# Performance work log

Hardware: AMD Instinct MI355X
Metric: run time of the kernel (lower is better)

Reference implementation:

```python
import jax, jax.numpy as jnp
import numpy as np

B, N, D = 2, 2048, 768
H = 12
DH = D // H
SCALE = DH ** -0.5


def setup_inputs() -> dict:
    key = jax.random.key(0)
    k1, k2, k3 = jax.random.split(key, 3)
    x = jax.random.normal(k1, (B, N, D), dtype=jnp.float32)
    w_qkv = jax.random.normal(k2, (D, 3 * D), dtype=jnp.float32) * (D ** -0.5)
    b_qkv = jnp.zeros((3 * D,), dtype=jnp.float32)
    w_proj = jax.random.normal(k3, (D, D), dtype=jnp.float32) * (D ** -0.5)
    b_proj = jnp.zeros((D,), dtype=jnp.float32)
    return {"x": x, "w_qkv": w_qkv, "b_qkv": b_qkv, "w_proj": w_proj, "b_proj": b_proj}


def reference(x, w_qkv, b_qkv, w_proj, b_proj):
    b, n, d = x.shape
    # qkv: (B, n, 3, H, DH) -> (3, B, H, n, DH)
    qkv = (x @ w_qkv + b_qkv).reshape(b, n, 3, H, DH).transpose(2, 0, 3, 1, 4)
    q, k, v = qkv[0], qkv[1], qkv[2]
    # naive full attention matrix (B, H, n, n)
    attn = jnp.einsum('bhqd,bhkd->bhqk', q, k) * SCALE
    attn = jax.nn.softmax(attn, axis=-1)
    out = jnp.einsum('bhqk,bhkd->bhqd', attn, v)  # (B, H, n, DH)
    out = out.transpose(0, 2, 1, 3).reshape(b, n, d)
    return out @ w_proj + b_proj
```

## Files before the change

### kernel.cpp

```cpp
#include <hip/hip_runtime.h>


#define CB 2
#define CN 2048
#define CD 768
#define CH 12
#define CDH 64
#define CEXPSCALE 0.18033688f

typedef __bf16 bf16x8 __attribute__((ext_vector_type(8)));
typedef float f32x4 __attribute__((ext_vector_type(4)));
typedef unsigned short u16x8 __attribute__((ext_vector_type(8)));

static __device__ __forceinline__ unsigned short f2bf(float f) {
  union { float f; unsigned u; } v; v.f = f;
  unsigned r = v.u + 0x7fffu + ((v.u >> 16) & 1u);
  return (unsigned short)(r >> 16);
}

static __device__ __forceinline__ void gld_lds16(const unsigned short* g, unsigned short* lds_base) {
  __builtin_amdgcn_global_load_lds(
      (const __attribute__((address_space(1))) unsigned int*)g,
      (__attribute__((address_space(3))) unsigned int*)(unsigned int)(unsigned long long)lds_base,
      16, 0, 0);
}

__global__ __launch_bounds__(256) void prep(const float* __restrict__ x,
                                            unsigned short* __restrict__ xb,
                                            const float* __restrict__ w_qkv,
                                            unsigned short* __restrict__ wqkv_t,
                                            const float* __restrict__ w_proj,
                                            unsigned short* __restrict__ wproj_t) {
  __shared__ __align__(16) unsigned short t[64][72];
  const int bid = blockIdx.x, tid = threadIdx.x;
#pragma unroll
  for (int it = 0; it < 2; ++it) {
    size_t i = ((size_t)(bid * 2 + it) * 256 + tid) * 8;
    f32x4 a = *(const f32x4*)&x[i];
    f32x4 b = *(const f32x4*)&x[i + 4];
    u16x8 o;
#pragma unroll
    for (int j = 0; j < 4; ++j) { o[j] = f2bf(a[j]); o[4 + j] = f2bf(b[j]); }
    *(u16x8*)&xb[i] = o;
  }
  if (bid >= 576) return;
  const float* src; unsigned short* dst; int R, C, c0, r0;
  if (bid < 432) { src = w_qkv; dst = wqkv_t; R = 768; C = 2304; c0 = (bid % 36) * 64; r0 = (bid / 36) * 64; }
  else { int u = bid - 432; src = w_proj; dst = wproj_t; R = 768; C = 768; c0 = (u % 12) * 64; r0 = (u / 12) * 64; }
#pragma unroll
  for (int i = 0; i < 4; ++i) {
    int c = tid + i * 256;
    int row = c >> 4, cc = (c & 15) * 4;
    f32x4 v = *(const f32x4*)&src[(size_t)(r0 + row) * C + c0 + cc];
#pragma unroll
    for (int j = 0; j < 4; ++j) t[row][cc + j] = f2bf(v[j]);
  }
  __syncthreads();
#pragma unroll
  for (int i = 0; i < 2; ++i) {
    int c = tid + i * 256;
    int drow = c >> 3, rc = (c & 7) * 8;
    u16x8 v;
#pragma unroll
    for (int j = 0; j < 8; ++j) v[j] = t[rc + j][drow];
    *(u16x8*)&dst[(size_t)(c0 + drow) * R + r0 + rc] = v;
  }
}

extern __shared__ __align__(16) unsigned short smem[];

template <int TM, int TN>
__global__ __launch_bounds__(256, 4) void gemm_db(const unsigned short* __restrict__ A,
                                                  const unsigned short* __restrict__ Bt,
                                                  const float* __restrict__ bias,
                                                  int M, int N, int K, int mode,
                                                  unsigned short* __restrict__ o0,
                                                  unsigned short* __restrict__ o1,
                                                  unsigned short* __restrict__ o2,
                                                  float* __restrict__ outF) {
  constexpr int NT = TN / 32;
  unsigned short* As = smem;
  unsigned short* Bs = smem + 2 * TM * 32;
  unsigned short* Ct = smem;
  const int tid = threadIdx.x;
  const int w = tid >> 6, lane = tid & 63, quad = lane >> 4, lc = lane & 15;
  const int wm = (w >> 1) * 32, wn = (w & 1) * (TN / 2);
  const int row0 = blockIdx.y * TM, col0 = blockIdx.x * TN;
  f32x4 acc[2][NT] = {};

  const int rl = lane >> 2, cl = lane & 3;
  const int gc = cl ^ ((rl >> 1) & 3);
  const int rsw = (lc >> 1) & 3;
  const int nk = K / 32;

  auto stage = [&](int kt, int buf) {
    const int k0 = kt * 32;
    gld_lds16(&A[(size_t)(row0 + w * 16 + rl) * K + k0 + gc * 8],
              &As[buf * (TM * 32) + (w * 16) * 32]);
#pragma unroll
    for (int jb = 0; jb < TN / 64; ++jb)
      gld_lds16(&Bt[(size_t)(col0 + w * (TN / 4) + jb * 16 + rl) * K + k0 + gc * 8],
                &Bs[buf * (TN * 32) + (w * (TN / 4) + jb * 16) * 32]);
  };

  stage(0, 0);
  for (int kt = 0; kt < nk; ++kt) {
    const int bb = kt & 1;
    __syncthreads();
    if (kt + 1 < nk) stage(kt + 1, bb ^ 1);
    bf16x8 af[2], bfv[NT];
#pragma unroll
    for (int mt = 0; mt < 2; ++mt)
      af[mt] = *(const bf16x8*)&As[bb * (TM * 32) + (wm + mt * 16 + lc) * 32 + (quad ^ rsw) * 8];
#pragma unroll
    for (int nt = 0; nt < NT; ++nt)
      bfv[nt] = *(const bf16x8*)&Bs[bb * (TN * 32) + (wn + nt * 16 + lc) * 32 + (quad ^ rsw) * 8];
#pragma unroll
    for (int mt = 0; mt < 2; ++mt)
#pragma unroll
      for (int nt = 0; nt < NT; ++nt)
        acc[mt][nt] = __builtin_amdgcn_mfma_f32_16x16x32_bf16(af[mt], bfv[nt], acc[mt][nt], 0, 0, 0);
  }

  if (mode == 0 && col0 >= 1536) {
    __syncthreads();
#pragma unroll
    for (int mt = 0; mt < 2; ++mt) {
#pragma unroll
      for (int nt = 0; nt < NT; ++nt) {
        int jl = wn + nt * 16 + lc;
        int il0 = wm + mt * 16 + quad * 4;
        float bj = bias[col0 + jl];
        unsigned short a0 = f2bf(acc[mt][nt][0] + bj);
        unsigned short a1 = f2bf(acc[mt][nt][1] + bj);
        unsigned short a2 = f2bf(acc[mt][nt][2] + bj);
        unsigned short a3 = f2bf(acc[mt][nt][3] + bj);
        uint2 dd;
        dd.x = (unsigned)a0 | ((unsigned)a1 << 16);
        dd.y = (unsigned)a2 | ((unsigned)a3 << 16);
        *(uint2*)&Ct[jl * (TM + 8) + il0] = dd;
      }
    }
    __syncthreads();
    const int b = row0 >> 11, n0 = row0 & 2047;
    constexpr int CPR = TM / 8;
#pragma unroll
    for (int i = 0; i < (TN * CPR) / 256; ++i) {
      int c = tid + i * 256;
      int jl = c / CPR, cc = (c % CPR) * 8;
      u16x8 v = *(const u16x8*)&Ct[jl * (TM + 8) + cc];
      int jcol = col0 - 1536 + jl;
      int h = jcol >> 6, d = jcol & 63;
      size_t gr = ((size_t)(b * CH + h) * CDH + d);
      *(u16x8*)&o2[gr * CN + n0 + cc] = v;
    }
  } else {
#pragma unroll
    for (int mt = 0; mt < 2; ++mt) {
#pragma unroll
      for (int nt = 0; nt < NT; ++nt) {
#pragma unroll
        for (int r = 0; r < 4; ++r) {
          int i = row0 + wm + mt * 16 + quad * 4 + r;
          int j = col0 + wn + nt * 16 + lc;
          float v = acc[mt][nt][r] + bias[j];
          if (mode == 0) {
            int b = i >> 11, n = i & 2047;
            int sec = (j >= 768) ? 1 : 0;
            int within = j - sec * 768;
            int h = within >> 6, d = within & 63;
            int bh = b * CH + h;
            if (sec == 0) o0[((size_t)bh * CN + n) * CDH + d] = f2bf(v * CEXPSCALE);
            else          o1[((size_t)bh * CN + n) * CDH + d] = f2bf(v);
          } else {
            outF[(size_t)i * N + j] = v;
          }
        }
      }
    }
  }
}

__global__ __launch_bounds__(256, 3) void attn64(const unsigned short* __restrict__ Q,
                                                 const unsigned short* __restrict__ K,
                                                 const unsigned short* __restrict__ Vt,
                                                 unsigned short* __restrict__ O) {
  __shared__ __align__(16) unsigned short Kls[2][64 * 64];
  __shared__ __align__(16) unsigned short Vls[2][64 * 64];
  __shared__ __align__(16) unsigned short P[4][16][88];
  const int bh = blockIdx.x, qt = blockIdx.y;
  const int tid = threadIdx.x;
  const int w = tid >> 6, lane = tid & 63, quad = lane >> 4, lc = lane & 15;
  const unsigned short* Qb = Q + (size_t)bh * CN * CDH;
  const unsigned short* Kb = K + (size_t)bh * CN * CDH;
  const unsigned short* Vb = Vt + (size_t)bh * CDH * CN;
  const int q0 = qt * 64 + w * 16;

  const int sr = lane >> 3, sc = lane & 7;
  const int sg = sc ^ sr;
  const int ksw = lc & 7;
  const int c0r = quad ^ ksw;
  const int c1r = c0r ^ 4;

  bf16x8 qf0 = *(const bf16x8*)&Qb[(size_t)(q0 + lc) * CDH + quad * 8];
  bf16x8 qf1 = *(const bf16x8*)&Qb[(size_t)(q0 + lc) * CDH + 32 + quad * 8];

  f32x4 o[4] = {};
  float rs = 0.f;

#pragma unroll
  for (int j2 = 0; j2 < 2; ++j2) {
    int j = w * 2 + j2;
    int r = j * 8 + sr;
    gld_lds16(&Kb[(size_t)r * CDH + sg * 8], &Kls[0][j * 8 * 64]);
    gld_lds16(&Vb[(size_t)r * CN + 0 + sg * 8], &Vls[0][j * 8 * 64]);
  }

  for (int kt = 0; kt < CN / 64; ++kt) {
    const int bb = kt & 1;
    __syncthreads();
    if (kt + 1 < CN / 64) {
      const int kn = (kt + 1) * 64;
#pragma unroll
      for (int j2 = 0; j2 < 2; ++j2) {
        int j = w * 2 + j2;
        int r = j * 8 + sr;
        gld_lds16(&Kb[(size_t)(kn + r) * CDH + sg * 8], &Kls[bb ^ 1][j * 8 * 64]);
        gld_lds16(&Vb[(size_t)r * CN + kn + sg * 8], &Vls[bb ^ 1][j * 8 * 64]);
      }
    }
#pragma unroll
    for (int t = 0; t < 4; ++t) {
      bf16x8 kf0 = *(const bf16x8*)&Kls[bb][(t * 16 + lc) * 64 + c0r * 8];
      bf16x8 kf1 = *(const bf16x8*)&Kls[bb][(t * 16 + lc) * 64 + c1r * 8];
      f32x4 z = {0.f, 0.f, 0.f, 0.f};
      z = __builtin_amdgcn_mfma_f32_16x16x32_bf16(kf0, qf0, z, 0, 0, 0);
      z = __builtin_amdgcn_mfma_f32_16x16x32_bf16(kf1, qf1, z, 0, 0, 0);
      float p0 = exp2f(z[0]);
      float p1 = exp2f(z[1]);
      float p2 = exp2f(z[2]);
      float p3 = exp2f(z[3]);
      rs += (p0 + p1) + (p2 + p3);
      unsigned d0 = __builtin_amdgcn_perm(__float_as_uint(p1), __float_as_uint(p0), 0x07060302u);
      unsigned d1 = __builtin_amdgcn_perm(__float_as_uint(p3), __float_as_uint(p2), 0x07060302u);
      uint2 dd; dd.x = d0; dd.y = d1;
      *(uint2*)&P[w][lc][t * 16 + quad * 4] = dd;
    }
    asm volatile("s_waitcnt lgkmcnt(0)" ::: "memory");
    bf16x8 pf0 = *(const bf16x8*)&P[w][lc][quad * 8];
    bf16x8 pf1 = *(const bf16x8*)&P[w][lc][32 + quad * 8];
#pragma unroll
    for (int dt = 0; dt < 4; ++dt) {
      bf16x8 vf0 = *(const bf16x8*)&Vls[bb][(dt * 16 + lc) * 64 + c0r * 8];
      bf16x8 vf1 = *(const bf16x8*)&Vls[bb][(dt * 16 + lc) * 64 + c1r * 8];
      o[dt] = __builtin_amdgcn_mfma_f32_16x16x32_bf16(pf0, vf0, o[dt], 0, 0, 0);
      o[dt] = __builtin_amdgcn_mfma_f32_16x16x32_bf16(pf1, vf1, o[dt], 0, 0, 0);
    }
  }

  rs += __shfl_xor(rs, 16, 64);
  rs += __shfl_xor(rs, 32, 64);
  const int b = bh / CH, h = bh - b * CH;
#pragma unroll
  for (int r = 0; r < 4; ++r) {
    float lr = __shfl(rs, quad * 4 + r, 64);
    float inv = 1.0f / lr;
#pragma unroll
    for (int dt = 0; dt < 4; ++dt) {
      int i = b * CN + q0 + quad * 4 + r;
      int j = h * CDH + dt * 16 + lc;
      O[(size_t)i * CD + j] = f2bf(o[dt][r] * inv);
    }
  }
}

extern "C" void kernel_launch(void* const* d_in, const int* in_sizes, int n_in,
                              void* d_out, int out_size, void* d_ws, size_t ws_size,
                              hipStream_t stream) {
  const float* x      = (const float*)d_in[0];
  const float* w_qkv  = (const float*)d_in[1];
  const float* b_qkv  = (const float*)d_in[2];
  const float* w_proj = (const float*)d_in[3];
  const float* b_proj = (const float*)d_in[4];
  float* out = (float*)d_out;
  unsigned short* ws = (unsigned short*)d_ws;

  unsigned short* xb      = ws;
  unsigned short* wqkv_t  = xb + (size_t)4096 * 768;
  unsigned short* wproj_t = wqkv_t + (size_t)2304 * 768;
  unsigned short* Qs  = wproj_t + (size_t)768 * 768;
  unsigned short* Ks  = Qs  + (size_t)CB * CH * CN * CDH;
  unsigned short* Vts = Ks  + (size_t)CB * CH * CN * CDH;
  unsigned short* AO  = Vts + (size_t)CB * CH * CN * CDH;

  const size_t smem_qkv  = (size_t)2 * (64 + 128) * 32 * 2;
  const size_t smem_proj = (size_t)2 * (64 + 64) * 32 * 2;

  prep<<<768, 256, 0, stream>>>(x, xb, w_qkv, wqkv_t, w_proj, wproj_t);
  gemm_db<64, 128><<<dim3(2304 / 128, 4096 / 64), 256, smem_qkv, stream>>>(
      xb, wqkv_t, b_qkv, 4096, 2304, 768, 0, Qs, Ks, Vts, nullptr);
  attn64<<<dim3(CB * CH, CN / 64), 256, 0, stream>>>(Qs, Ks, Vts, AO);
  gemm_db<64, 64><<<dim3(768 / 64, 4096 / 64), 256, smem_proj, stream>>>(
      AO, wproj_t, b_proj, 4096, 768, 768, 1, nullptr, nullptr, nullptr, out);
}
```

Measured before the change: 169.6 us.

## Split attention tile 2x2 across waves to share K/V fragments

Each wave now handles 32 queries against half of each 64-key tile, instead of 16 queries against all 64 keys. Each K and V fragment read from LDS now feeds two query subtiles, halving shared-memory reads per MFMA. The two key-half partial outputs and row sums are combined at the end through LDS, with an extra barrier. This adds more accumulator registers and an epilogue reduction.

```diff
diff --git a/kernel.cpp b/kernel.cpp
--- a/kernel.cpp
+++ b/kernel.cpp
@@ -185,91 +185,132 @@
                                                  const unsigned short* __restrict__ K,
                                                  const unsigned short* __restrict__ Vt,
                                                  unsigned short* __restrict__ O) {
-  __shared__ __align__(16) unsigned short Kls[2][64 * 64];
-  __shared__ __align__(16) unsigned short Vls[2][64 * 64];
-  __shared__ __align__(16) unsigned short P[4][16][88];
+  __shared__ __align__(16) unsigned short KV[4 * 4096];
+  __shared__ __align__(16) unsigned short P[4][32 * 48];
   const int bh = blockIdx.x, qt = blockIdx.y;
   const int tid = threadIdx.x;
   const int w = tid >> 6, lane = tid & 63, quad = lane >> 4, lc = lane & 15;
+  const int qh = w >> 1, kh = w & 1;
   const unsigned short* Qb = Q + (size_t)bh * CN * CDH;
   const unsigned short* Kb = K + (size_t)bh * CN * CDH;
   const unsigned short* Vb = Vt + (size_t)bh * CDH * CN;
-  const int q0 = qt * 64 + w * 16;
+  const int q0 = qt * 64 + qh * 32;
 
   const int sr = lane >> 3, sc = lane & 7;
   const int sg = sc ^ sr;
   const int ksw = lc & 7;
   const int c0r = quad ^ ksw;
   const int c1r = c0r ^ 4;
-
-  bf16x8 qf0 = *(const bf16x8*)&Qb[(size_t)(q0 + lc) * CDH + quad * 8];
-  bf16x8 qf1 = *(const bf16x8*)&Qb[(size_t)(q0 + lc) * CDH + 32 + quad * 8];
-
-  f32x4 o[4] = {};
-  float rs = 0.f;
+  const int vcr = (kh * 4 + quad) ^ ksw;
+
+  bf16x8 qf[2][2];
+#pragma unroll
+  for (int s = 0; s < 2; ++s) {
+    qf[s][0] = *(const bf16x8*)&Qb[(size_t)(q0 + s * 16 + lc) * CDH + quad * 8];
+    qf[s][1] = *(const bf16x8*)&Qb[(size_t)(q0 + s * 16 + lc) * CDH + 32 + quad * 8];
+  }
+
+  f32x4 o[2][4] = {};
+  float rs[2] = {0.f, 0.f};
 
 #pragma unroll
   for (int j2 = 0; j2 < 2; ++j2) {
     int j = w * 2 + j2;
     int r = j * 8 + sr;
-    gld_lds16(&Kb[(size_t)r * CDH + sg * 8], &Kls[0][j * 8 * 64]);
-    gld_lds16(&Vb[(size_t)r * CN + 0 + sg * 8], &Vls[0][j * 8 * 64]);
+    gld_lds16(&Kb[(size_t)r * CDH + sg * 8], &KV[j * 8 * 64]);
+    gld_lds16(&Vb[(size_t)r * CN + 0 + sg * 8], &KV[8192 + j * 8 * 64]);
   }
 
   for (int kt = 0; kt < CN / 64; ++kt) {
     const int bb = kt & 1;
+    const int kbase = bb * 4096;
+    const int vbase = 8192 + bb * 4096;
     __syncthreads();
     if (kt + 1 < CN / 64) {
       const int kn = (kt + 1) * 64;
+      const int kbn = (bb ^ 1) * 4096;
+      const int vbn = 8192 + (bb ^ 1) * 4096;
 #pragma unroll
       for (int j2 = 0; j2 < 2; ++j2) {
         int j = w * 2 + j2;
         int r = j * 8 + sr;
-        gld_lds16(&Kb[(size_t)(kn + r) * CDH + sg * 8], &Kls[bb ^ 1][j * 8 * 64]);
-        gld_lds16(&Vb[(size_t)r * CN + kn + sg * 8], &Vls[bb ^ 1][j * 8 * 64]);
-      }
-    }
-#pragma unroll
-    for (int t = 0; t < 4; ++t) {
-      bf16x8 kf0 = *(const bf16x8*)&Kls[bb][(t * 16 + lc) * 64 + c0r * 8];
-      bf16x8 kf1 = *(const bf16x8*)&Kls[bb][(t * 16 + lc) * 64 + c1r * 8];
-      f32x4 z = {0.f, 0.f, 0.f, 0.f};
-      z = __builtin_amdgcn_mfma_f32_16x16x32_bf16(kf0, qf0, z, 0, 0, 0);
-      z = __builtin_amdgcn_mfma_f32_16x16x32_bf16(kf1, qf1, z, 0, 0, 0);
-      float p0 = exp2f(z[0]);
-      float p1 = exp2f(z[1]);
-      float p2 = exp2f(z[2]);
-      float p3 = exp2f(z[3]);
-      rs += (p0 + p1) + (p2 + p3);
-      unsigned d0 = __builtin_amdgcn_perm(__float_as_uint(p1), __float_as_uint(p0), 0x07060302u);
-      unsigned d1 = __builtin_amdgcn_perm(__float_as_uint(p3), __float_as_uint(p2), 0x07060302u);
-      uint2 dd; dd.x = d0; dd.y = d1;
-      *(uint2*)&P[w][lc][t * 16 + quad * 4] = dd;
+        gld_lds16(&Kb[(size_t)(kn + r) * CDH + sg * 8], &KV[kbn + j * 8 * 64]);
+        gld_lds16(&Vb[(size_t)r * CN + kn + sg * 8], &KV[vbn + j * 8 * 64]);
+      }
+    }
+#pragma unroll
+    for (int ks = 0; ks < 2; ++ks) {
+      const int krow = kh * 32 + ks * 16 + lc;
+      bf16x8 kf0 = *(const bf16x8*)&KV[kbase + krow * 64 + c0r * 8];
+      bf16x8 kf1 = *(const bf16x8*)&KV[kbase + krow * 64 + c1r * 8];
+#pragma unroll
+      for (int s = 0; s < 2; ++s) {
+        f32x4 z = {0.f, 0.f, 0.f, 0.f};
+        z = __builtin_amdgcn_mfma_f32_16x16x32_bf16(kf0, qf[s][0], z, 0, 0, 0);
+        z = __builtin_amdgcn_mfma_f32_16x16x32_bf16(kf1, qf[s][1], z, 0, 0, 0);
+        float p0 = exp2f(z[0]);
+        float p1 = exp2f(z[1]);
+        float p2 = exp2f(z[2]);
+        float p3 = exp2f(z[3]);
+        rs[s] += (p0 + p1) + (p2 + p3);
+        unsigned d0 = __builtin_amdgcn_perm(__float_as_uint(p1), __float_as_uint(p0), 0x07060302u);
+        unsigned d1 = __builtin_amdgcn_perm(__float_as_uint(p3), __float_as_uint(p2), 0x07060302u);
+        uint2 dd; dd.x = d0; dd.y = d1;
+        *(uint2*)&P[w][(s * 16 + lc) * 48 + ks * 16 + quad * 4] = dd;
+      }
     }
     asm volatile("s_waitcnt lgkmcnt(0)" ::: "memory");
-    bf16x8 pf0 = *(const bf16x8*)&P[w][lc][quad * 8];
-    bf16x8 pf1 = *(const bf16x8*)&P[w][lc][32 + quad * 8];
+    bf16x8 pf[2];
+#pragma unroll
+    for (int s = 0; s < 2; ++s)
+      pf[s] = *(const bf16x8*)&P[w][(s * 16 + lc) * 48 + quad * 8];
 #pragma unroll
     for (int dt = 0; dt < 4; ++dt) {
-      bf16x8 vf0 = *(const bf16x8*)&Vls[bb][(dt * 16 + lc) * 64 + c0r * 8];
-      bf16x8 vf1 = *(const bf16x8*)&Vls[bb][(dt * 16 + lc) * 64 + c1r * 8];
-      o[dt] = __builtin_amdgcn_mfma_f32_16x16x32_bf16(pf0, vf0, o[dt], 0, 0, 0);
-      o[dt] = __builtin_amdgcn_mfma_f32_16x16x32_bf16(pf1, vf1, o[dt], 0, 0, 0);
-    }
-  }
-
-  rs += __shfl_xor(rs, 16, 64);
-  rs += __shfl_xor(rs, 32, 64);
-  const int b = bh / CH, h = bh - b * CH;
-#pragma unroll
-  for (int r = 0; r < 4; ++r) {
-    float lr = __shfl(rs, quad * 4 + r, 64);
-    float inv = 1.0f / lr;
-#pragma unroll
-    for (int dt = 0; dt < 4; ++dt) {
-      int i = b * CN + q0 + quad * 4 + r;
-      int j = h * CDH + dt * 16 + lc;
-      O[(size_t)i * CD + j] = f2bf(o[dt][r] * inv);
+      bf16x8 vf = *(const bf16x8*)&KV[vbase + (dt * 16 + lc) * 64 + vcr * 8];
+#pragma unroll
+      for (int s = 0; s < 2; ++s)
+        o[s][dt] = __builtin_amdgcn_mfma_f32_16x16x32_bf16(pf[s], vf, o[s][dt], 0, 0, 0);
+    }
+  }
+
+#pragma unroll
+  for (int s = 0; s < 2; ++s) {
+    rs[s] += __shfl_xor(rs[s], 16, 64);
+    rs[s] += __shfl_xor(rs[s], 32, 64);
+  }
+
+  float* ex = (float*)KV;
+  float* rs_lds = (float*)((char*)KV + 2 * 64 * 36 * 4);
+  __syncthreads();
+  if (kh == 1) {
+#pragma unroll
+    for (int dt = 0; dt < 4; ++dt)
+#pragma unroll
+      for (int s = 0; s < 2; ++s)
+        *(f32x4*)&ex[(qh * 64 + dt * 16 + lc) * 36 + s * 16 + quad * 4] = o[s][dt];
+    if (quad == 0) {
+      rs_lds[qh * 32 + lc] = rs[0];
+      rs_lds[qh * 32 + 16 + lc] = rs[1];
+    }
+  }
+  __syncthreads();
+  if (kh == 0) {
+    const int b = bh / CH, h = bh - b * CH;
+#pragma unroll
+    for (int s = 0; s < 2; ++s) {
+      float lt = rs[s] + rs_lds[qh * 32 + s * 16 + lc];
+#pragma unroll
+      for (int r = 0; r < 4; ++r) {
+        float lr = __shfl(lt, quad * 4 + r, 64);
+        float inv = 1.0f / lr;
+#pragma unroll
+        for (int dt = 0; dt < 4; ++dt) {
+          f32x4 part = *(const f32x4*)&ex[(qh * 64 + dt * 16 + lc) * 36 + s * 16 + quad * 4];
+          int i = b * CN + q0 + s * 16 + quad * 4 + r;
+          int j = h * CDH + dt * 16 + lc;
+          O[(size_t)i * CD + j] = f2bf((o[s][dt][r] + part[r]) * inv);
+        }
+      }
     }
   }
 }
```

Result: slower. 177.4 us (+4.6%).
